# Optimization experiments

Hardware: AMD Instinct MI355X
Metric: run time of the kernel (lower is better)

The kernel has to match this reference:

```python
import jax, jax.numpy as jnp
import numpy as np

B, S, E, HEADS, LATENT = 8, 4096, 2048, 16, 64
HEAD_SIZE = E // HEADS  # 128
NEG = -1e20


def setup_inputs() -> dict:
    key = jax.random.key(0)
    k0, k1, k2, k3, k4 = jax.random.split(key, 5)
    return {
        "x": jax.random.normal(k0, (B, S, E), dtype=jnp.float32) * 0.02,
        "W_dkv": jax.random.normal(k1, (LATENT, E), dtype=jnp.float32) * 0.02,
        "W_k": jax.random.normal(k2, (HEAD_SIZE, LATENT), dtype=jnp.float32) * 0.02,
        "W_v": jax.random.normal(k3, (HEAD_SIZE, LATENT), dtype=jnp.float32) * 0.02,
        "W_q": jax.random.normal(k4, (HEAD_SIZE, E), dtype=jnp.float32) * 0.02,
    }


def reference(x, W_dkv, W_k, W_v, W_q):
    # x: [B,S,E]; nn.Linear computes x @ W.T (weight layout [out,in])
    head_size = W_k.shape[0]
    latent = jnp.einsum("bse,le->bsl", x, W_dkv)        # latent KV cache [B,S,L]
    absorbed_q = W_q.T @ W_k                              # [E,H] @ [H,L] -> [E,L]
    q_res = jnp.einsum("bse,el->bsl", x, absorbed_q)     # [B,S,L]
    scale = head_size ** -0.5
    scores = jnp.einsum("bql,bkl->bqk", q_res, latent) * scale  # [B,S,S]
    seq = x.shape[1]
    causal = jnp.tril(jnp.ones((seq, seq), dtype=bool))
    scores = jnp.where(causal, scores, NEG)
    attn = jax.nn.softmax(scores, axis=-1)               # dropout skipped (eval mode)
    v = jnp.einsum("bsl,hl->bsh", latent, W_v)           # compressed V [B,S,H]
    out = jnp.einsum("bqk,bkh->bqh", attn, v)            # [B,S,head_size]
    return out, latent  # latent == kv_cache returned by the module
```

## Files before the change

kernel.cpp:

```cpp
#include <hip/hip_runtime.h>
#include <hip/hip_bf16.h>

#define NB 8
#define NS 4096
#define NE 2048
#define NL 64
#define NH 128
#define NM (NB*NS)

typedef unsigned short ushort_t;
typedef __attribute__((ext_vector_type(4))) float f32x4;
typedef __attribute__((ext_vector_type(8))) __bf16 bf16x8;
typedef __attribute__((ext_vector_type(8))) unsigned short u16x8;
typedef __attribute__((ext_vector_type(4))) unsigned short u16x4;

#define SCALE2 0.1275174537f

__device__ __forceinline__ float fast_exp2(float x) {
    return __builtin_amdgcn_exp2f(x);
}

__device__ __forceinline__ unsigned short f2bf(float f) {
    union { float f; unsigned u; } v; v.f = f;
    unsigned u = v.u + 0x7fffu + ((v.u >> 16) & 1u);
    return (unsigned short)(u >> 16);
}

__device__ __forceinline__ float bf2f(ushort_t u) {
    union { unsigned u; float f; } v; v.u = (unsigned)u << 16; return v.f;
}

__device__ __forceinline__ int swz(int row, int colbyte) {
    return (row * 128 + colbyte) ^ ((row & 7) << 4);
}

__device__ __forceinline__ void wg_barrier() {
    asm volatile("s_waitcnt lgkmcnt(0)" ::: "memory");
    __builtin_amdgcn_s_barrier();
    __builtin_amdgcn_sched_barrier(0);
}

__global__ __launch_bounds__(256) void prep_kernel(
    const float* __restrict__ Wdkv, const float* __restrict__ Wk,
    const float* __restrict__ Wq, ushort_t* __restrict__ WcatT)
{
    __shared__ float wk[128 * 64];
    const int t = threadIdx.x;
    for (int i = t; i < 128 * 64; i += 256) wk[i] = Wk[i];
    __syncthreads();
    const int e = blockIdx.x * 256 + t;
    const int l0 = blockIdx.y * 16;
    float acc[16];
    #pragma unroll
    for (int l = 0; l < 16; ++l) acc[l] = 0.f;
    for (int h = 0; h < 128; ++h) {
        float q = Wq[h * NE + e];
        #pragma unroll
        for (int l = 0; l < 16; ++l) acc[l] += q * wk[h * 64 + l0 + l];
    }
    for (int l = 0; l < 16; ++l) WcatT[(64 + l0 + l) * NE + e] = f2bf(acc[l] * SCALE2);
    for (int l = 0; l < 16; ++l) WcatT[(l0 + l) * NE + e] = f2bf(Wdkv[(l0 + l) * NE + e]);
}

__global__ __launch_bounds__(256) void proj_kernel(
    const float* __restrict__ x, const ushort_t* __restrict__ WcatT,
    float* __restrict__ latent_out, ushort_t* __restrict__ k_bf,
    ushort_t* __restrict__ q_bf, ushort_t* __restrict__ kt)
{
    __shared__ ushort_t As[2][64 * 64];
    __shared__ ushort_t Bs[2][128 * 64];
    const int tid = threadIdx.x;
    const int w = tid >> 6, lane = tid & 63, lg = lane >> 4, li = lane & 15;
    const int m0 = blockIdx.x * 64;
    const int wm = (w >> 1) * 32, wn = (w & 1) * 64;
    const int srow = tid >> 3, scol = tid & 7;

    f32x4 acc[2][4];
    #pragma unroll
    for (int i = 0; i < 2; ++i)
        #pragma unroll
        for (int j = 0; j < 4; ++j) acc[i][j] = f32x4{0.f, 0.f, 0.f, 0.f};

    f32x4 a0reg[2][2], a1reg[2][2];
    u16x8 b0reg[4], b1reg[4];

#define PLOAD(k0, AR, BR) do { \
    _Pragma("unroll") for (int p = 0; p < 2; ++p) { \
        const float* gp = x + (long)(m0 + srow + 32 * p) * NE + (k0) + scol * 8; \
        AR[p][0] = *reinterpret_cast<const f32x4*>(gp); \
        AR[p][1] = *reinterpret_cast<const f32x4*>(gp + 4); } \
    _Pragma("unroll") for (int p = 0; p < 4; ++p) \
        BR[p] = *reinterpret_cast<const u16x8*>(WcatT + (long)(srow + 32 * p) * NE + (k0) + scol * 8); \
} while (0)

#define PWRITE(AR, BR, buf) do { \
    _Pragma("unroll") for (int p = 0; p < 2; ++p) { \
        union { unsigned uw[4]; u16x8 v; } hu; \
        asm("v_cvt_pk_bf16_f32 %0, %1, %2" : "=v"(hu.uw[0]) : "v"(AR[p][0][0]), "v"(AR[p][0][1])); \
        asm("v_cvt_pk_bf16_f32 %0, %1, %2" : "=v"(hu.uw[1]) : "v"(AR[p][0][2]), "v"(AR[p][0][3])); \
        asm("v_cvt_pk_bf16_f32 %0, %1, %2" : "=v"(hu.uw[2]) : "v"(AR[p][1][0]), "v"(AR[p][1][1])); \
        asm("v_cvt_pk_bf16_f32 %0, %1, %2" : "=v"(hu.uw[3]) : "v"(AR[p][1][2]), "v"(AR[p][1][3])); \
        *reinterpret_cast<u16x8*>(reinterpret_cast<char*>(As[buf]) + swz(srow + 32 * p, scol * 16)) = hu.v; } \
    _Pragma("unroll") for (int p = 0; p < 4; ++p) \
        *reinterpret_cast<u16x8*>(reinterpret_cast<char*>(Bs[buf]) + swz(srow + 32 * p, scol * 16)) = BR[p]; \
} while (0)

    auto compute = [&](int buf) {
        #pragma unroll
        for (int c = 0; c < 2; ++c) {
            bf16x8 af[2], bfv[4];
            #pragma unroll
            for (int mf = 0; mf < 2; ++mf)
                af[mf] = *reinterpret_cast<const bf16x8*>(
                    reinterpret_cast<const char*>(As[buf]) + swz(wm + 16 * mf + li, c * 64 + lg * 16));
            #pragma unroll
            for (int nf = 0; nf < 4; ++nf)
                bfv[nf] = *reinterpret_cast<const bf16x8*>(
                    reinterpret_cast<const char*>(Bs[buf]) + swz(wn + 16 * nf + li, c * 64 + lg * 16));
            #pragma unroll
            for (int mf = 0; mf < 2; ++mf)
                #pragma unroll
                for (int nf = 0; nf < 4; ++nf)
                    acc[mf][nf] = __builtin_amdgcn_mfma_f32_16x16x32_bf16(
                        af[mf], bfv[nf], acc[mf][nf], 0, 0, 0);
        }
    };

    PLOAD(0, a0reg, b0reg);
    PLOAD(64, a1reg, b1reg);
    PWRITE(a0reg, b0reg, 0);
    wg_barrier();

    for (int ks = 0; ks < 32; ks += 2) {
        if (ks + 2 < 32) PLOAD((ks + 2) * 64, a0reg, b0reg);
        compute(0);
        PWRITE(a1reg, b1reg, 1);
        wg_barrier();
        if (ks + 3 < 32) PLOAD((ks + 3) * 64, a1reg, b1reg);
        compute(1);
        if (ks + 2 < 32) PWRITE(a0reg, b0reg, 0);
        wg_barrier();
    }

    const int b = m0 >> 12, s0 = m0 & 4095;
    #pragma unroll
    for (int mf = 0; mf < 2; ++mf) {
        #pragma unroll
        for (int nf = 0; nf < 4; ++nf) {
            int col = wn + 16 * nf + li;
            #pragma unroll
            for (int r = 0; r < 4; ++r) {
                int row = m0 + wm + 16 * mf + 4 * lg + r;
                float v = acc[mf][nf][r];
                if (wn == 0) {
                    latent_out[(long)row * NL + col] = v;
                    k_bf[(long)row * NL + col] = f2bf(v);
                    *reinterpret_cast<ushort_t*>(reinterpret_cast<char*>(As[0]) +
                        swz(wm + 16 * mf + 4 * lg + r, col * 2)) = f2bf(v);
                } else {
                    q_bf[(long)row * NL + (col - 64)] = f2bf(v);
                }
            }
        }
    }
    wg_barrier();
    union { u16x8 u; bf16x8 v; } iu;
    #pragma unroll
    for (int j = 0; j < 8; ++j)
        iu.u[j] = (lg == (li >> 3) + 2 * (w & 1) && (li & 7) == j)
                      ? (ushort_t)0x3F80 : (ushort_t)0;
    const int ckt = w >> 1;
    f32x4 ktacc[4];
    #pragma unroll
    for (int nf = 0; nf < 4; ++nf) {
        bf16x8 bfv = *reinterpret_cast<const bf16x8*>(
            reinterpret_cast<const char*>(As[0]) + swz(16 * nf + li, ckt * 64 + lg * 16));
        ktacc[nf] = __builtin_amdgcn_mfma_f32_16x16x32_bf16(
            iu.v, bfv, f32x4{0.f, 0.f, 0.f, 0.f}, 0, 0, 0);
    }
    #pragma unroll
    for (int nf = 0; nf < 4; ++nf)
        #pragma unroll
        for (int r = 0; r < 4; ++r)
            kt[(long)(b * 64 + 16 * w + 4 * lg + r) * NS + s0 + 16 * nf + li] =
                f2bf(ktacc[nf][r]);
}

__global__ __launch_bounds__(256, 2) void attn_kernel(
    const ushort_t* __restrict__ q_bf, const ushort_t* __restrict__ k_bf,
    const ushort_t* __restrict__ kt, const float* __restrict__ Wv,
    float* __restrict__ out)
{
    __shared__ __attribute__((aligned(16))) char smem[65536];
    ushort_t* OW = (ushort_t*)smem;
    float* mw = (float*)(smem + 32768);
    float* lw = (float*)(smem + 33792);
    ushort_t* Ms = (ushort_t*)(smem + 36864);
    ushort_t* Wvs = (ushort_t*)(smem + 45056);
    float* Os = (float*)smem;

    const int tid = threadIdx.x;
    const int w = tid >> 6, lane = tid & 63, lg = lane >> 4, li = lane & 15;
    const int l = blockIdx.x;
    const int b = l & 7;
    const int p_ = l >> 3;
    const int k_ = p_ >> 1, e_ = p_ & 1, kk = (k_ & 15) * 2;
    const int qt = (k_ >> 4) ? (e_ ? kk + 1 : 63 - kk) : (e_ ? 62 - kk : kk);
    const int Q0 = qt << 6;
    const int nch = (qt >> 1) + 1;

    const int krow = tid >> 1, khalf = tid & 1;
    const int trow = tid >> 2, tkq = (tid & 3) * 32;

    bf16x8 qf[4][2];
    #pragma unroll
    for (int qb = 0; qb < 4; ++qb)
        #pragma unroll
        for (int c = 0; c < 2; ++c)
            qf[qb][c] = *reinterpret_cast<const bf16x8*>(
                q_bf + ((long)b * NS + Q0 + 16 * qb + li) * NL + c * 32 + lg * 8);

    float m_r[4], l_r[4];
    #pragma unroll
    for (int qb = 0; qb < 4; ++qb) { m_r[qb] = -1.0e30f; l_r[qb] = 0.f; }
    f32x4 oacc[4][4];
    #pragma unroll
    for (int qb = 0; qb < 4; ++qb)
        #pragma unroll
        for (int n = 0; n < 4; ++n) oacc[qb][n] = f32x4{0.f, 0.f, 0.f, 0.f};

    u16x8 k0reg[4], t0reg[4], k1reg[4], t1reg[4];

#define ALOAD(ch, KR, TR) do { \
    const int kv0_ = (ch) * 128; \
    _Pragma("unroll") for (int pp = 0; pp < 4; ++pp) \
        KR[pp] = *reinterpret_cast<const u16x8*>( \
            k_bf + ((long)b * NS + kv0_ + krow) * NL + khalf * 32 + pp * 8); \
    _Pragma("unroll") for (int pp = 0; pp < 4; ++pp) \
        TR[pp] = *reinterpret_cast<const u16x8*>( \
            kt + ((long)b * 64 + trow) * NS + kv0_ + tkq + pp * 8); \
} while (0)

#define AWRITE(KR, TR, buf) do { \
    char* Kb_ = smem + (buf) * 16384; \
    char* Tb_ = smem + 32768 + (buf) * 16384; \
    _Pragma("unroll") for (int pp = 0; pp < 4; ++pp) \
        *reinterpret_cast<u16x8*>(Kb_ + swz(krow, khalf * 64 + pp * 16)) = KR[pp]; \
    _Pragma("unroll") for (int pp = 0; pp < 4; ++pp) { \
        const int kv8 = tkq + pp * 8; \
        const int colp = (kv8 & 0x60) | ((kv8 & 0xC) << 1) | ((kv8 & 0x10) >> 2); \
        const int xo = (trow & 15) << 4; \
        u16x4 lo = {TR[pp][0], TR[pp][1], TR[pp][2], TR[pp][3]}; \
        u16x4 hi = {TR[pp][4], TR[pp][5], TR[pp][6], TR[pp][7]}; \
        *reinterpret_cast<u16x4*>(Tb_ + trow * 256 + ((colp * 2) ^ xo)) = lo; \
        *reinterpret_cast<u16x4*>(Tb_ + trow * 256 + (((colp + 8) * 2) ^ xo)) = hi; \
    } \
} while (0)

    auto compute = [&](int buf, bool diag, int kv0) {
        const char* Kb = smem + buf * 16384;
        const char* Tb = smem + 32768 + buf * 16384;
        f32x4 s[2][4];
        #pragma unroll
        for (int kvb = 0; kvb < 2; ++kvb)
            #pragma unroll
            for (int qb = 0; qb < 4; ++qb) s[kvb][qb] = f32x4{0.f, 0.f, 0.f, 0.f};
        __builtin_amdgcn_s_setprio(1);
        #pragma unroll
        for (int c = 0; c < 2; ++c)
            #pragma unroll
            for (int kvb = 0; kvb < 2; ++kvb) {
                bf16x8 a = *reinterpret_cast<const bf16x8*>(
                    Kb + swz(32 * w + 16 * kvb + li, c * 64 + lg * 16));
                #pragma unroll
                for (int qb = 0; qb < 4; ++qb)
                    s[kvb][qb] = __builtin_amdgcn_mfma_f32_16x16x32_bf16(
                        a, qf[qb][c], s[kvb][qb], 0, 0, 0);
            }
        __builtin_amdgcn_s_setprio(0);
        if (diag) {
            #pragma unroll
            for (int kvb = 0; kvb < 2; ++kvb)
                #pragma unroll
                for (int qb = 0; qb < 4; ++qb)
                    #pragma unroll
                    for (int r = 0; r < 4; ++r) {
                        int kv_g = kv0 + 32 * w + 16 * kvb + 4 * lg + r;
                        int q_g = Q0 + 16 * qb + li;
                        if (kv_g > q_g) s[kvb][qb][r] = -3.0e38f;
                    }
        }
        float mx[4];
        #pragma unroll
        for (int qb = 0; qb < 4; ++qb) {
            float m0_ = fmaxf(fmaxf(s[0][qb][0], s[0][qb][1]), fmaxf(s[0][qb][2], s[0][qb][3]));
            float m1_ = fmaxf(fmaxf(s[1][qb][0], s[1][qb][1]), fmaxf(s[1][qb][2], s[1][qb][3]));
            mx[qb] = fmaxf(m0_, m1_);
        }
        bool ok = (mx[0] <= m_r[0] + 8.f) && (mx[1] <= m_r[1] + 8.f) &&
                  (mx[2] <= m_r[2] + 8.f) && (mx[3] <= m_r[3] + 8.f);
        if (!__all(ok)) {
            #pragma unroll
            for (int qb = 0; qb < 4; ++qb) {
                float mxf = fmaxf(mx[qb], __shfl_xor(mx[qb], 16));
                mxf = fmaxf(mxf, __shfl_xor(mxf, 32));
                float m_new = fmaxf(m_r[qb], mxf);
                float corr = fast_exp2(m_r[qb] - m_new);
                m_r[qb] = m_new;
                l_r[qb] *= corr;
                float corrO[4];
                #pragma unroll
                for (int r = 0; r < 4; ++r)
                    corrO[r] = __shfl(corr, (lane & 48) | (4 * lg + r));
                #pragma unroll
                for (int n = 0; n < 4; ++n)
                    #pragma unroll
                    for (int r = 0; r < 4; ++r) oacc[qb][n][r] *= corrO[r];
            }
        }
        #pragma unroll
        for (int qb = 0; qb < 4; ++qb) {
            float rs = 0.f;
            #pragma unroll
            for (int kvb = 0; kvb < 2; ++kvb)
                #pragma unroll
                for (int r = 0; r < 4; ++r) {
                    float pv = fast_exp2(s[kvb][qb][r] - m_r[qb]);
                    s[kvb][qb][r] = pv;
                    rs += pv;
                }
            l_r[qb] += rs;
        }
        bf16x8 vb[4];
        #pragma unroll
        for (int n = 0; n < 4; ++n)
            vb[n] = *reinterpret_cast<const bf16x8*>(
                Tb + (16 * n + li) * 256 + ((64 * w + 16 * lg) ^ (li << 4)));
        __builtin_amdgcn_s_setprio(1);
        #pragma unroll
        for (int qb = 0; qb < 4; ++qb) {
            union { unsigned uw[4]; bf16x8 v; } pa;
            asm("v_cvt_pk_bf16_f32 %0, %1, %2" : "=v"(pa.uw[0]) : "v"(s[0][qb][0]), "v"(s[0][qb][1]));
            asm("v_cvt_pk_bf16_f32 %0, %1, %2" : "=v"(pa.uw[1]) : "v"(s[0][qb][2]), "v"(s[0][qb][3]));
            asm("v_cvt_pk_bf16_f32 %0, %1, %2" : "=v"(pa.uw[2]) : "v"(s[1][qb][0]), "v"(s[1][qb][1]));
            asm("v_cvt_pk_bf16_f32 %0, %1, %2" : "=v"(pa.uw[3]) : "v"(s[1][qb][2]), "v"(s[1][qb][3]));
            #pragma unroll
            for (int n = 0; n < 4; ++n)
                oacc[qb][n] = __builtin_amdgcn_mfma_f32_16x16x32_bf16(
                    pa.v, vb[n], oacc[qb][n], 0, 0, 0);
        }
        __builtin_amdgcn_s_setprio(0);
    };

    ALOAD(0, k0reg, t0reg);
    if (nch >= 2) ALOAD(1, k1reg, t1reg);
    AWRITE(k0reg, t0reg, 0);
    wg_barrier();
    for (int i = 0; i < nch; i += 2) {
        if (i + 2 < nch) ALOAD(i + 2, k0reg, t0reg);
        compute(0, i == nch - 1, i * 128);
        if (i + 1 < nch) AWRITE(k1reg, t1reg, 1);
        wg_barrier();
        if (i + 1 >= nch) break;
        if (i + 3 < nch) ALOAD(i + 3, k1reg, t1reg);
        compute(1, i + 1 == nch - 1, (i + 1) * 128);
        if (i + 2 < nch) AWRITE(k0reg, t0reg, 0);
        wg_barrier();
    }

    #pragma unroll
    for (int qb = 0; qb < 4; ++qb) {
        l_r[qb] += __shfl_xor(l_r[qb], 16);
        l_r[qb] += __shfl_xor(l_r[qb], 32);
    }
    if (lg == 0) {
        #pragma unroll
        for (int qb = 0; qb < 4; ++qb) {
            mw[w * 64 + 16 * qb + li] = m_r[qb];
            lw[w * 64 + 16 * qb + li] = l_r[qb];
        }
    }
    #pragma unroll
    for (int qb = 0; qb < 4; ++qb)
        #pragma unroll
        for (int r = 0; r < 4; ++r) {
            union { unsigned uw[2]; u16x4 v; } u;
            asm("v_cvt_pk_bf16_f32 %0, %1, %2" : "=v"(u.uw[0]) : "v"(oacc[qb][0][r]), "v"(oacc[qb][1][r]));
            asm("v_cvt_pk_bf16_f32 %0, %1, %2" : "=v"(u.uw[1]) : "v"(oacc[qb][2][r]), "v"(oacc[qb][3][r]));
            int q = 16 * qb + 4 * lg + r;
            *reinterpret_cast<u16x4*>(OW + (w * 64 + q) * 64 + li * 4) = u.v;
        }
    wg_barrier();

    {
        const int q = tid >> 2, g = tid & 3;
        float m4[4], l4[4];
        #pragma unroll
        for (int ww = 0; ww < 4; ++ww) { m4[ww] = mw[ww * 64 + q]; l4[ww] = lw[ww * 64 + q]; }
        float M = fmaxf(fmaxf(m4[0], m4[1]), fmaxf(m4[2], m4[3]));
        float cw[4], L = 0.f;
        #pragma unroll
        for (int ww = 0; ww < 4; ++ww) { cw[ww] = fast_exp2(m4[ww] - M); L += cw[ww] * l4[ww]; }
        float inv = 1.f / L;
        float merged[16];
        #pragma unroll
        for (int e = 0; e < 16; ++e) {
            float a = 0.f;
            #pragma unroll
            for (int ww = 0; ww < 4; ++ww)
                a += cw[ww] * bf2f(OW[(ww * 64 + q) * 64 + e * 4 + g]);
            merged[e] = a * inv;
        }
        #pragma unroll
        for (int ee = 0; ee < 8; ++ee) {
            unsigned pk;
            asm("v_cvt_pk_bf16_f32 %0, %1, %2" : "=v"(pk) : "v"(merged[2 * ee]), "v"(merged[2 * ee + 1]));
            *reinterpret_cast<unsigned*>(reinterpret_cast<char*>(Ms) + swz(q, g * 32 + 4 * ee)) = pk;
        }
        const int r = tid >> 1, hf = tid & 1;
        const float* wp = Wv + r * 64 + hf * 32;
        #pragma unroll
        for (int qq = 0; qq < 2; ++qq) {
            f32x4 w0 = *reinterpret_cast<const f32x4*>(wp + qq * 16);
            f32x4 w1 = *reinterpret_cast<const f32x4*>(wp + qq * 16 + 4);
            f32x4 w2 = *reinterpret_cast<const f32x4*>(wp + qq * 16 + 8);
            f32x4 w3 = *reinterpret_cast<const f32x4*>(wp + qq * 16 + 12);
            u16x8 h0, h1;
            #pragma unroll
            for (int jj = 0; jj < 4; ++jj) {
                h0[jj] = f2bf(w0[jj]); h0[4 + jj] = f2bf(w1[jj]);
                h1[jj] = f2bf(w2[jj]); h1[4 + jj] = f2bf(w3[jj]);
            }
            *reinterpret_cast<u16x8*>(reinterpret_cast<char*>(Wvs) + swz(r, hf * 64 + qq * 32)) = h0;
            *reinterpret_cast<u16x8*>(reinterpret_cast<char*>(Wvs) + swz(r, hf * 64 + qq * 32 + 16)) = h1;
        }
    }
    wg_barrier();

    f32x4 vacc[2][4];
    #pragma unroll
    for (int i = 0; i < 2; ++i)
        #pragma unroll
        for (int j = 0; j < 4; ++j) vacc[i][j] = f32x4{0.f, 0.f, 0.f, 0.f};
    #pragma unroll
    for (int c = 0; c < 2; ++c) {
        bf16x8 af[2], bfv[4];
        #pragma unroll
        for (int mf = 0; mf < 2; ++mf)
            af[mf] = *reinterpret_cast<const bf16x8*>(
                reinterpret_cast<const char*>(Wvs) + swz(32 * w + 16 * mf + li, c * 64 + lg * 16));
        #pragma unroll
        for (int nf = 0; nf < 4; ++nf)
            bfv[nf] = *reinterpret_cast<const bf16x8*>(
                reinterpret_cast<const char*>(Ms) + swz(16 * nf + li, c * 64 + lg * 16));
        #pragma unroll
        for (int mf = 0; mf < 2; ++mf)
            #pragma unroll
            for (int nf = 0; nf < 4; ++nf)
                vacc[mf][nf] = __builtin_amdgcn_mfma_f32_16x16x32_bf16(
                    af[mf], bfv[nf], vacc[mf][nf], 0, 0, 0);
    }
    wg_barrier();
    #pragma unroll
    for (int mf = 0; mf < 2; ++mf)
        #pragma unroll
        for (int nf = 0; nf < 4; ++nf)
            #pragma unroll
            for (int r = 0; r < 4; ++r)
                Os[(16 * nf + li) * 132 + 32 * w + 16 * mf + 4 * lg + r] = vacc[mf][nf][r];
    wg_barrier();
    {
        const int r = tid >> 2, cb = (tid & 3) * 32;
        float* op = out + ((long)b * NS + Q0 + r) * NH + cb;
        const float* sp = Os + r * 132 + cb;
        #pragma unroll
        for (int qq = 0; qq < 8; ++qq)
            *reinterpret_cast<f32x4*>(op + 4 * qq) = *reinterpret_cast<const f32x4*>(sp + 4 * qq);
    }
}

extern "C" void kernel_launch(void* const* d_in, const int* in_sizes, int n_in,
                              void* d_out, int out_size, void* d_ws, size_t ws_size,
                              hipStream_t stream) {
    const float* x    = (const float*)d_in[0];
    const float* Wdkv = (const float*)d_in[1];
    const float* Wk   = (const float*)d_in[2];
    const float* Wv   = (const float*)d_in[3];
    const float* Wq   = (const float*)d_in[4];

    float* out = (float*)d_out;
    float* latent_out = out + (long)NM * NH;

    ushort_t* WcatT = (ushort_t*)d_ws;
    ushort_t* q_bf  = WcatT + 128 * NE;
    ushort_t* k_bf  = q_bf + (long)NM * NL;
    ushort_t* kt    = k_bf + (long)NM * NL;

    hipLaunchKernelGGL(prep_kernel, dim3(NE / 256, 4), dim3(256), 0, stream, Wdkv, Wk, Wq, WcatT);
    hipLaunchKernelGGL(proj_kernel, dim3(NM / 64), dim3(256), 0, stream,
                       x, WcatT, latent_out, k_bf, q_bf, kt);
    hipLaunchKernelGGL(attn_kernel, dim3(512), dim3(256), 0, stream,
                       q_bf, k_bf, kt, Wv, out);
}
```

Measured before the change: 133.4 us.

## Load K fragments directly into registers, drop K and Wv LDS staging

```diff
diff --git a/kernel.cpp b/kernel.cpp
--- a/kernel.cpp
+++ b/kernel.cpp
@@ -191,12 +191,11 @@
     const ushort_t* __restrict__ kt, const float* __restrict__ Wv,
     float* __restrict__ out)
 {
-    __shared__ __attribute__((aligned(16))) char smem[65536];
+    __shared__ __attribute__((aligned(16))) char smem[45056];
     ushort_t* OW = (ushort_t*)smem;
     float* mw = (float*)(smem + 32768);
     float* lw = (float*)(smem + 33792);
     ushort_t* Ms = (ushort_t*)(smem + 36864);
-    ushort_t* Wvs = (ushort_t*)(smem + 45056);
     float* Os = (float*)smem;
 
     const int tid = threadIdx.x;
@@ -209,7 +208,6 @@
     const int Q0 = qt << 6;
     const int nch = (qt >> 1) + 1;
 
-    const int krow = tid >> 1, khalf = tid & 1;
     const int trow = tid >> 2, tkq = (tid & 3) * 32;
 
     bf16x8 qf[4][2];
@@ -229,37 +227,39 @@
         #pragma unroll
         for (int n = 0; n < 4; ++n) oacc[qb][n] = f32x4{0.f, 0.f, 0.f, 0.f};
 
-    u16x8 k0reg[4], t0reg[4], k1reg[4], t1reg[4];
-
-#define ALOAD(ch, KR, TR) do { \
+    bf16x8 kfA[2][2], kfB[2][2];
+    u16x8 treg[4];
+
+#define KLOAD(ch, KF) do { \
+    const int kv0_ = (ch) * 128; \
+    _Pragma("unroll") for (int c = 0; c < 2; ++c) \
+        _Pragma("unroll") for (int kvb = 0; kvb < 2; ++kvb) \
+            KF[c][kvb] = *reinterpret_cast<const bf16x8*>( \
+                k_bf + ((long)b * NS + kv0_ + 32 * w + 16 * kvb + li) * NL + c * 32 + lg * 8); \
+} while (0)
+
+#define TLOAD(ch) do { \
     const int kv0_ = (ch) * 128; \
     _Pragma("unroll") for (int pp = 0; pp < 4; ++pp) \
-        KR[pp] = *reinterpret_cast<const u16x8*>( \
-            k_bf + ((long)b * NS + kv0_ + krow) * NL + khalf * 32 + pp * 8); \
-    _Pragma("unroll") for (int pp = 0; pp < 4; ++pp) \
-        TR[pp] = *reinterpret_cast<const u16x8*>( \
+        treg[pp] = *reinterpret_cast<const u16x8*>( \
             kt + ((long)b * 64 + trow) * NS + kv0_ + tkq + pp * 8); \
 } while (0)
 
-#define AWRITE(KR, TR, buf) do { \
-    char* Kb_ = smem + (buf) * 16384; \
-    char* Tb_ = smem + 32768 + (buf) * 16384; \
-    _Pragma("unroll") for (int pp = 0; pp < 4; ++pp) \
-        *reinterpret_cast<u16x8*>(Kb_ + swz(krow, khalf * 64 + pp * 16)) = KR[pp]; \
+#define TWRITE(buf) do { \
+    char* Tb_ = smem + (buf) * 16384; \
     _Pragma("unroll") for (int pp = 0; pp < 4; ++pp) { \
         const int kv8 = tkq + pp * 8; \
         const int colp = (kv8 & 0x60) | ((kv8 & 0xC) << 1) | ((kv8 & 0x10) >> 2); \
         const int xo = (trow & 15) << 4; \
-        u16x4 lo = {TR[pp][0], TR[pp][1], TR[pp][2], TR[pp][3]}; \
-        u16x4 hi = {TR[pp][4], TR[pp][5], TR[pp][6], TR[pp][7]}; \
+        u16x4 lo = {treg[pp][0], treg[pp][1], treg[pp][2], treg[pp][3]}; \
+        u16x4 hi = {treg[pp][4], treg[pp][5], treg[pp][6], treg[pp][7]}; \
         *reinterpret_cast<u16x4*>(Tb_ + trow * 256 + ((colp * 2) ^ xo)) = lo; \
         *reinterpret_cast<u16x4*>(Tb_ + trow * 256 + (((colp + 8) * 2) ^ xo)) = hi; \
     } \
 } while (0)
 
-    auto compute = [&](int buf, bool diag, int kv0) {
-        const char* Kb = smem + buf * 16384;
-        const char* Tb = smem + 32768 + buf * 16384;
+    auto compute = [&](int buf, bool diag, int kv0, bf16x8 (&kf)[2][2]) {
+        const char* Tb = smem + buf * 16384;
         f32x4 s[2][4];
         #pragma unroll
         for (int kvb = 0; kvb < 2; ++kvb)
@@ -270,12 +270,10 @@
         for (int c = 0; c < 2; ++c)
             #pragma unroll
             for (int kvb = 0; kvb < 2; ++kvb) {
-                bf16x8 a = *reinterpret_cast<const bf16x8*>(
-                    Kb + swz(32 * w + 16 * kvb + li, c * 64 + lg * 16));
                 #pragma unroll
                 for (int qb = 0; qb < 4; ++qb)
                     s[kvb][qb] = __builtin_amdgcn_mfma_f32_16x16x32_bf16(
-                        a, qf[qb][c], s[kvb][qb], 0, 0, 0);
+                        kf[c][kvb], qf[qb][c], s[kvb][qb], 0, 0, 0);
             }
         __builtin_amdgcn_s_setprio(0);
         if (diag) {
@@ -352,21 +350,42 @@
         __builtin_amdgcn_s_setprio(0);
     };
 
-    ALOAD(0, k0reg, t0reg);
-    if (nch >= 2) ALOAD(1, k1reg, t1reg);
-    AWRITE(k0reg, t0reg, 0);
-    wg_barrier();
+    KLOAD(0, kfA);
+    TLOAD(0);
+    if (nch >= 2) KLOAD(1, kfB);
+    TWRITE(0);
+    if (nch >= 2) TLOAD(1);
+    wg_barrier();
+
     for (int i = 0; i < nch; i += 2) {
-        if (i + 2 < nch) ALOAD(i + 2, k0reg, t0reg);
-        compute(0, i == nch - 1, i * 128);
-        if (i + 1 < nch) AWRITE(k1reg, t1reg, 1);
+        compute(0, i == nch - 1, i * 128, kfA);
+        if (i + 2 < nch) KLOAD(i + 2, kfA);
+        if (i + 1 < nch) TWRITE(1);
+        if (i + 2 < nch) TLOAD(i + 2);
         wg_barrier();
         if (i + 1 >= nch) break;
-        if (i + 3 < nch) ALOAD(i + 3, k1reg, t1reg);
-        compute(1, i + 1 == nch - 1, (i + 1) * 128);
-        if (i + 2 < nch) AWRITE(k0reg, t0reg, 0);
+        compute(1, i + 1 == nch - 1, (i + 1) * 128, kfB);
+        if (i + 3 < nch) KLOAD(i + 3, kfB);
+        if (i + 2 < nch) TWRITE(0);
+        if (i + 3 < nch) TLOAD(i + 3);
         wg_barrier();
     }
+
+    bf16x8 waf[2][2];
+    #pragma unroll
+    for (int c = 0; c < 2; ++c)
+        #pragma unroll
+        for (int mf = 0; mf < 2; ++mf) {
+            const float* wp_ = Wv + (32 * w + 16 * mf + li) * 64 + c * 32 + lg * 8;
+            f32x4 wa = *reinterpret_cast<const f32x4*>(wp_);
+            f32x4 wb = *reinterpret_cast<const f32x4*>(wp_ + 4);
+            union { unsigned uw[4]; bf16x8 v; } hu;
+            asm("v_cvt_pk_bf16_f32 %0, %1, %2" : "=v"(hu.uw[0]) : "v"(wa[0]), "v"(wa[1]));
+            asm("v_cvt_pk_bf16_f32 %0, %1, %2" : "=v"(hu.uw[1]) : "v"(wa[2]), "v"(wa[3]));
+            asm("v_cvt_pk_bf16_f32 %0, %1, %2" : "=v"(hu.uw[2]) : "v"(wb[0]), "v"(wb[1]));
+            asm("v_cvt_pk_bf16_f32 %0, %1, %2" : "=v"(hu.uw[3]) : "v"(wb[2]), "v"(wb[3]));
+            waf[c][mf] = hu.v;
+        }
 
     #pragma unroll
     for (int qb = 0; qb < 4; ++qb) {
@@ -417,23 +436,6 @@
             asm("v_cvt_pk_bf16_f32 %0, %1, %2" : "=v"(pk) : "v"(merged[2 * ee]), "v"(merged[2 * ee + 1]));
             *reinterpret_cast<unsigned*>(reinterpret_cast<char*>(Ms) + swz(q, g * 32 + 4 * ee)) = pk;
         }
-        const int r = tid >> 1, hf = tid & 1;
-        const float* wp = Wv + r * 64 + hf * 32;
-        #pragma unroll
-        for (int qq = 0; qq < 2; ++qq) {
-            f32x4 w0 = *reinterpret_cast<const f32x4*>(wp + qq * 16);
-            f32x4 w1 = *reinterpret_cast<const f32x4*>(wp + qq * 16 + 4);
-            f32x4 w2 = *reinterpret_cast<const f32x4*>(wp + qq * 16 + 8);
-            f32x4 w3 = *reinterpret_cast<const f32x4*>(wp + qq * 16 + 12);
-            u16x8 h0, h1;
-            #pragma unroll
-            for (int jj = 0; jj < 4; ++jj) {
-                h0[jj] = f2bf(w0[jj]); h0[4 + jj] = f2bf(w1[jj]);
-                h1[jj] = f2bf(w2[jj]); h1[4 + jj] = f2bf(w3[jj]);
-            }
-            *reinterpret_cast<u16x8*>(reinterpret_cast<char*>(Wvs) + swz(r, hf * 64 + qq * 32)) = h0;
-            *reinterpret_cast<u16x8*>(reinterpret_cast<char*>(Wvs) + swz(r, hf * 64 + qq * 32 + 16)) = h1;
-        }
     }
     wg_barrier();
 
@@ -444,11 +446,7 @@
         for (int j = 0; j < 4; ++j) vacc[i][j] = f32x4{0.f, 0.f, 0.f, 0.f};
     #pragma unroll
     for (int c = 0; c < 2; ++c) {
-        bf16x8 af[2], bfv[4];
-        #pragma unroll
-        for (int mf = 0; mf < 2; ++mf)
-            af[mf] = *reinterpret_cast<const bf16x8*>(
-                reinterpret_cast<const char*>(Wvs) + swz(32 * w + 16 * mf + li, c * 64 + lg * 16));
+        bf16x8 bfv[4];
         #pragma unroll
         for (int nf = 0; nf < 4; ++nf)
             bfv[nf] = *reinterpret_cast<const bf16x8*>(
@@ -458,7 +456,7 @@
             #pragma unroll
             for (int nf = 0; nf < 4; ++nf)
                 vacc[mf][nf] = __builtin_amdgcn_mfma_f32_16x16x32_bf16(
-                    af[mf], bfv[nf], vacc[mf][nf], 0, 0, 0);
+                    waf[c][mf], bfv[nf], vacc[mf][nf], 0, 0, 0);
     }
     wg_barrier();
     #pragma unroll
```

New measurement: 139.5 us. +4.6%, slower.

## Split causal KV range across two blocks and add a separate merge kernel

Applied to the files above, without the earlier changes.

```diff
diff --git a/kernel.cpp b/kernel.cpp
--- a/kernel.cpp
+++ b/kernel.cpp
@@ -188,26 +188,23 @@
 
 __global__ __launch_bounds__(256, 2) void attn_kernel(
     const ushort_t* __restrict__ q_bf, const ushort_t* __restrict__ k_bf,
-    const ushort_t* __restrict__ kt, const float* __restrict__ Wv,
-    float* __restrict__ out)
+    const ushort_t* __restrict__ kt, unsigned* __restrict__ Opart,
+    float* __restrict__ lpart, float* __restrict__ mpart)
 {
     __shared__ __attribute__((aligned(16))) char smem[65536];
     ushort_t* OW = (ushort_t*)smem;
     float* mw = (float*)(smem + 32768);
     float* lw = (float*)(smem + 33792);
-    ushort_t* Ms = (ushort_t*)(smem + 36864);
-    ushort_t* Wvs = (ushort_t*)(smem + 45056);
-    float* Os = (float*)smem;
 
     const int tid = threadIdx.x;
     const int w = tid >> 6, lane = tid & 63, lg = lane >> 4, li = lane & 15;
-    const int l = blockIdx.x;
-    const int b = l & 7;
-    const int p_ = l >> 3;
-    const int k_ = p_ >> 1, e_ = p_ & 1, kk = (k_ & 15) * 2;
-    const int qt = (k_ >> 4) ? (e_ ? kk + 1 : 63 - kk) : (e_ ? 62 - kk : kk);
+    const int j = blockIdx.x;
+    const int qt = 63 - (j >> 4);
+    const int b = j & 7;
+    const int h = (j >> 3) & 1;
     const int Q0 = qt << 6;
-    const int nch = (qt >> 1) + 1;
+    const int ntot = (qt >> 1) + 1;
+    const int nch = (ntot - h + 1) >> 1;
 
     const int krow = tid >> 1, khalf = tid & 1;
     const int trow = tid >> 2, tkq = (tid & 3) * 32;
@@ -352,20 +349,24 @@
         __builtin_amdgcn_s_setprio(0);
     };
 
-    ALOAD(0, k0reg, t0reg);
-    if (nch >= 2) ALOAD(1, k1reg, t1reg);
-    AWRITE(k0reg, t0reg, 0);
-    wg_barrier();
-    for (int i = 0; i < nch; i += 2) {
-        if (i + 2 < nch) ALOAD(i + 2, k0reg, t0reg);
-        compute(0, i == nch - 1, i * 128);
-        if (i + 1 < nch) AWRITE(k1reg, t1reg, 1);
+    if (nch > 0) {
+        ALOAD(h, k0reg, t0reg);
+        if (nch >= 2) ALOAD(h + 2, k1reg, t1reg);
+        AWRITE(k0reg, t0reg, 0);
         wg_barrier();
-        if (i + 1 >= nch) break;
-        if (i + 3 < nch) ALOAD(i + 3, k1reg, t1reg);
-        compute(1, i + 1 == nch - 1, (i + 1) * 128);
-        if (i + 2 < nch) AWRITE(k0reg, t0reg, 0);
-        wg_barrier();
+        for (int i = 0; i < nch; i += 2) {
+            const int c0_ = h + 2 * i;
+            if (i + 2 < nch) ALOAD(h + 2 * (i + 2), k0reg, t0reg);
+            compute(0, c0_ == ntot - 1, c0_ * 128);
+            if (i + 1 < nch) AWRITE(k1reg, t1reg, 1);
+            wg_barrier();
+            if (i + 1 >= nch) break;
+            const int c1_ = h + 2 * (i + 1);
+            if (i + 3 < nch) ALOAD(h + 2 * (i + 3), k1reg, t1reg);
+            compute(1, c1_ == ntot - 1, c1_ * 128);
+            if (i + 2 < nch) AWRITE(k0reg, t0reg, 0);
+            wg_barrier();
+        }
     }
 
     #pragma unroll
@@ -401,20 +402,66 @@
         float cw[4], L = 0.f;
         #pragma unroll
         for (int ww = 0; ww < 4; ++ww) { cw[ww] = fast_exp2(m4[ww] - M); L += cw[ww] * l4[ww]; }
-        float inv = 1.f / L;
-        float merged[16];
+        float numer[16];
         #pragma unroll
         for (int e = 0; e < 16; ++e) {
             float a = 0.f;
             #pragma unroll
             for (int ww = 0; ww < 4; ++ww)
                 a += cw[ww] * bf2f(OW[(ww * 64 + q) * 64 + e * 4 + g]);
-            merged[e] = a * inv;
-        }
+            numer[e] = a;
+        }
+        const long P = ((long)(h * NB + b) << 6) + qt;
+        unsigned* op = Opart + P * 2048 + q * 32 + g * 8;
         #pragma unroll
         for (int ee = 0; ee < 8; ++ee) {
             unsigned pk;
-            asm("v_cvt_pk_bf16_f32 %0, %1, %2" : "=v"(pk) : "v"(merged[2 * ee]), "v"(merged[2 * ee + 1]));
+            asm("v_cvt_pk_bf16_f32 %0, %1, %2" : "=v"(pk) : "v"(numer[2 * ee]), "v"(numer[2 * ee + 1]));
+            op[ee] = pk;
+        }
+        if (g == 0) {
+            lpart[P * 64 + q] = L;
+            mpart[P * 64 + q] = M;
+        }
+    }
+}
+
+__global__ __launch_bounds__(256) void merge_kernel(
+    const unsigned* __restrict__ Opart, const float* __restrict__ lpart,
+    const float* __restrict__ mpart, const float* __restrict__ Wv,
+    float* __restrict__ out)
+{
+    __shared__ __attribute__((aligned(16))) char smem[33792];
+    ushort_t* Ms = (ushort_t*)smem;
+    ushort_t* Wvs = (ushort_t*)(smem + 8192);
+    float* Os = (float*)smem;
+    const int blk = blockIdx.x;
+    const int b = blk & 7, qt = blk >> 3;
+    const int tid = threadIdx.x;
+    const int w = tid >> 6, lane = tid & 63, lg = lane >> 4, li = lane & 15;
+
+    {
+        const int q = tid >> 2, g = tid & 3;
+        const long P1 = ((long)b << 6) + qt;
+        const long P2 = ((long)(NB + b) << 6) + qt;
+        float l1 = lpart[P1 * 64 + q], m1 = mpart[P1 * 64 + q];
+        float l2 = lpart[P2 * 64 + q], m2 = mpart[P2 * 64 + q];
+        float M = fmaxf(m1, m2);
+        float w1 = fast_exp2(m1 - M), w2 = fast_exp2(m2 - M);
+        float inv = 1.f / (w1 * l1 + w2 * l2);
+        float a1 = w1 * inv, a2 = w2 * inv;
+        const unsigned* o1 = Opart + P1 * 2048 + q * 32 + g * 8;
+        const unsigned* o2 = Opart + P2 * 2048 + q * 32 + g * 8;
+        #pragma unroll
+        for (int ee = 0; ee < 8; ++ee) {
+            unsigned u1 = o1[ee], u2 = o2[ee];
+            union { unsigned u; float f; } c0, c1, d0, d1;
+            c0.u = u1 << 16; c1.u = u1 & 0xffff0000u;
+            d0.u = u2 << 16; d1.u = u2 & 0xffff0000u;
+            float rlo = a1 * c0.f + a2 * d0.f;
+            float rhi = a1 * c1.f + a2 * d1.f;
+            unsigned pk;
+            asm("v_cvt_pk_bf16_f32 %0, %1, %2" : "=v"(pk) : "v"(rlo), "v"(rhi));
             *reinterpret_cast<unsigned*>(reinterpret_cast<char*>(Ms) + swz(q, g * 32 + 4 * ee)) = pk;
         }
         const int r = tid >> 1, hf = tid & 1;
@@ -422,14 +469,14 @@
         #pragma unroll
         for (int qq = 0; qq < 2; ++qq) {
             f32x4 w0 = *reinterpret_cast<const f32x4*>(wp + qq * 16);
-            f32x4 w1 = *reinterpret_cast<const f32x4*>(wp + qq * 16 + 4);
-            f32x4 w2 = *reinterpret_cast<const f32x4*>(wp + qq * 16 + 8);
+            f32x4 wv1 = *reinterpret_cast<const f32x4*>(wp + qq * 16 + 4);
+            f32x4 w2v = *reinterpret_cast<const f32x4*>(wp + qq * 16 + 8);
             f32x4 w3 = *reinterpret_cast<const f32x4*>(wp + qq * 16 + 12);
             u16x8 h0, h1;
             #pragma unroll
             for (int jj = 0; jj < 4; ++jj) {
-                h0[jj] = f2bf(w0[jj]); h0[4 + jj] = f2bf(w1[jj]);
-                h1[jj] = f2bf(w2[jj]); h1[4 + jj] = f2bf(w3[jj]);
+                h0[jj] = f2bf(w0[jj]); h0[4 + jj] = f2bf(wv1[jj]);
+                h1[jj] = f2bf(w2v[jj]); h1[4 + jj] = f2bf(w3[jj]);
             }
             *reinterpret_cast<u16x8*>(reinterpret_cast<char*>(Wvs) + swz(r, hf * 64 + qq * 32)) = h0;
             *reinterpret_cast<u16x8*>(reinterpret_cast<char*>(Wvs) + swz(r, hf * 64 + qq * 32 + 16)) = h1;
@@ -441,7 +488,7 @@
     #pragma unroll
     for (int i = 0; i < 2; ++i)
         #pragma unroll
-        for (int j = 0; j < 4; ++j) vacc[i][j] = f32x4{0.f, 0.f, 0.f, 0.f};
+        for (int jj = 0; jj < 4; ++jj) vacc[i][jj] = f32x4{0.f, 0.f, 0.f, 0.f};
     #pragma unroll
     for (int c = 0; c < 2; ++c) {
         bf16x8 af[2], bfv[4];
@@ -471,7 +518,7 @@
     wg_barrier();
     {
         const int r = tid >> 2, cb = (tid & 3) * 32;
-        float* op = out + ((long)b * NS + Q0 + r) * NH + cb;
+        float* op = out + ((long)b * NS + qt * 64 + r) * NH + cb;
         const float* sp = Os + r * 132 + cb;
         #pragma unroll
         for (int qq = 0; qq < 8; ++qq)
@@ -495,10 +542,15 @@
     ushort_t* q_bf  = WcatT + 128 * NE;
     ushort_t* k_bf  = q_bf + (long)NM * NL;
     ushort_t* kt    = k_bf + (long)NM * NL;
+    unsigned* Opart = (unsigned*)(kt + (long)NM * NL);
+    float* lpart = (float*)(Opart + (long)1024 * 2048);
+    float* mpart = lpart + 1024 * 64;
 
     hipLaunchKernelGGL(prep_kernel, dim3(NE / 256, 4), dim3(256), 0, stream, Wdkv, Wk, Wq, WcatT);
     hipLaunchKernelGGL(proj_kernel, dim3(NM / 64), dim3(256), 0, stream,
                        x, WcatT, latent_out, k_bf, q_bf, kt);
-    hipLaunchKernelGGL(attn_kernel, dim3(512), dim3(256), 0, stream,
-                       q_bf, k_bf, kt, Wv, out);
-}
+    hipLaunchKernelGGL(attn_kernel, dim3(1024), dim3(256), 0, stream,
+                       q_bf, k_bf, kt, Opart, lpart, mpart);
+    hipLaunchKernelGGL(merge_kernel, dim3(512), dim3(256), 0, stream,
+                       Opart, lpart, mpart, Wv, out);
+}
```

After: 139.9 us. 1.05x slower.

## Split attention into LDS-free per-wave KV partitions with separate merge kernel

Applied to the files above, without the earlier changes.

```diff
diff --git a/kernel.cpp b/kernel.cpp
--- a/kernel.cpp
+++ b/kernel.cpp
@@ -13,6 +13,7 @@
 typedef __attribute__((ext_vector_type(8))) __bf16 bf16x8;
 typedef __attribute__((ext_vector_type(8))) unsigned short u16x8;
 typedef __attribute__((ext_vector_type(4))) unsigned short u16x4;
+typedef __attribute__((ext_vector_type(4))) unsigned int u32x4;
 
 #define SCALE2 0.1275174537f
 
@@ -186,122 +187,93 @@
                 f2bf(ktacc[nf][r]);
 }
 
-__global__ __launch_bounds__(256, 2) void attn_kernel(
+__global__ __launch_bounds__(256, 3) void attn_kernel(
     const ushort_t* __restrict__ q_bf, const ushort_t* __restrict__ k_bf,
-    const ushort_t* __restrict__ kt, const float* __restrict__ Wv,
-    float* __restrict__ out)
+    const ushort_t* __restrict__ kt, unsigned* __restrict__ Opart,
+    float* __restrict__ lpart, float* __restrict__ mpart)
 {
-    __shared__ __attribute__((aligned(16))) char smem[65536];
-    ushort_t* OW = (ushort_t*)smem;
-    float* mw = (float*)(smem + 32768);
-    float* lw = (float*)(smem + 33792);
-    ushort_t* Ms = (ushort_t*)(smem + 36864);
-    ushort_t* Wvs = (ushort_t*)(smem + 45056);
-    float* Os = (float*)smem;
-
     const int tid = threadIdx.x;
     const int w = tid >> 6, lane = tid & 63, lg = lane >> 4, li = lane & 15;
-    const int l = blockIdx.x;
-    const int b = l & 7;
-    const int p_ = l >> 3;
-    const int k_ = p_ >> 1, e_ = p_ & 1, kk = (k_ & 15) * 2;
-    const int qt = (k_ >> 4) ? (e_ ? kk + 1 : 63 - kk) : (e_ ? 62 - kk : kk);
-    const int Q0 = qt << 6;
-    const int nch = (qt >> 1) + 1;
-
-    const int krow = tid >> 1, khalf = tid & 1;
-    const int trow = tid >> 2, tkq = (tid & 3) * 32;
-
-    bf16x8 qf[4][2];
-    #pragma unroll
-    for (int qb = 0; qb < 4; ++qb)
+    const int j = blockIdx.x;
+    const int t = 127 - (j >> 3);
+    const int b = j & 7;
+    const int h = w;
+    const int Q0 = t << 5;
+    const int nch = (h <= t) ? ((t - h) >> 2) + 1 : 0;
+
+    bf16x8 qf[2][2];
+    #pragma unroll
+    for (int qb = 0; qb < 2; ++qb)
         #pragma unroll
         for (int c = 0; c < 2; ++c)
             qf[qb][c] = *reinterpret_cast<const bf16x8*>(
                 q_bf + ((long)b * NS + Q0 + 16 * qb + li) * NL + c * 32 + lg * 8);
 
-    float m_r[4], l_r[4];
-    #pragma unroll
-    for (int qb = 0; qb < 4; ++qb) { m_r[qb] = -1.0e30f; l_r[qb] = 0.f; }
-    f32x4 oacc[4][4];
-    #pragma unroll
-    for (int qb = 0; qb < 4; ++qb)
+    float m_r[2], l_r[2];
+    m_r[0] = m_r[1] = -1.0e30f;
+    l_r[0] = l_r[1] = 0.f;
+    f32x4 oacc[2][4];
+    #pragma unroll
+    for (int qb = 0; qb < 2; ++qb)
         #pragma unroll
         for (int n = 0; n < 4; ++n) oacc[qb][n] = f32x4{0.f, 0.f, 0.f, 0.f};
 
-    u16x8 k0reg[4], t0reg[4], k1reg[4], t1reg[4];
-
-#define ALOAD(ch, KR, TR) do { \
-    const int kv0_ = (ch) * 128; \
-    _Pragma("unroll") for (int pp = 0; pp < 4; ++pp) \
-        KR[pp] = *reinterpret_cast<const u16x8*>( \
-            k_bf + ((long)b * NS + kv0_ + krow) * NL + khalf * 32 + pp * 8); \
-    _Pragma("unroll") for (int pp = 0; pp < 4; ++pp) \
-        TR[pp] = *reinterpret_cast<const u16x8*>( \
-            kt + ((long)b * 64 + trow) * NS + kv0_ + tkq + pp * 8); \
-} while (0)
-
-#define AWRITE(KR, TR, buf) do { \
-    char* Kb_ = smem + (buf) * 16384; \
-    char* Tb_ = smem + 32768 + (buf) * 16384; \
-    _Pragma("unroll") for (int pp = 0; pp < 4; ++pp) \
-        *reinterpret_cast<u16x8*>(Kb_ + swz(krow, khalf * 64 + pp * 16)) = KR[pp]; \
-    _Pragma("unroll") for (int pp = 0; pp < 4; ++pp) { \
-        const int kv8 = tkq + pp * 8; \
-        const int colp = (kv8 & 0x60) | ((kv8 & 0xC) << 1) | ((kv8 & 0x10) >> 2); \
-        const int xo = (trow & 15) << 4; \
-        u16x4 lo = {TR[pp][0], TR[pp][1], TR[pp][2], TR[pp][3]}; \
-        u16x4 hi = {TR[pp][4], TR[pp][5], TR[pp][6], TR[pp][7]}; \
-        *reinterpret_cast<u16x4*>(Tb_ + trow * 256 + ((colp * 2) ^ xo)) = lo; \
-        *reinterpret_cast<u16x4*>(Tb_ + trow * 256 + (((colp + 8) * 2) ^ xo)) = hi; \
+    union VB { u16x4 h4[2]; bf16x8 v; };
+    bf16x8 kfA[2][2], kfB[2][2];
+    VB vbA[4], vbB[4];
+
+#define AKLOAD(ch, KF, VBv) do { \
+    const int kv0_ = (ch) * 32; \
+    _Pragma("unroll") for (int c = 0; c < 2; ++c) \
+        _Pragma("unroll") for (int f = 0; f < 2; ++f) \
+            KF[c][f] = *reinterpret_cast<const bf16x8*>( \
+                k_bf + ((long)b * NS + kv0_ + 16 * f + li) * NL + c * 32 + lg * 8); \
+    _Pragma("unroll") for (int n = 0; n < 4; ++n) { \
+        const ushort_t* kp_ = kt + ((long)b * 64 + 16 * n + li) * NS + kv0_ + 4 * lg; \
+        VBv[n].h4[0] = *reinterpret_cast<const u16x4*>(kp_); \
+        VBv[n].h4[1] = *reinterpret_cast<const u16x4*>(kp_ + 16); \
     } \
 } while (0)
 
-    auto compute = [&](int buf, bool diag, int kv0) {
-        const char* Kb = smem + buf * 16384;
-        const char* Tb = smem + 32768 + buf * 16384;
-        f32x4 s[2][4];
-        #pragma unroll
-        for (int kvb = 0; kvb < 2; ++kvb)
-            #pragma unroll
-            for (int qb = 0; qb < 4; ++qb) s[kvb][qb] = f32x4{0.f, 0.f, 0.f, 0.f};
+    auto compute = [&](bf16x8 (&kf)[2][2], VB (&vb)[4], bool diag, int kv0) {
+        f32x4 s[2][2];
+        #pragma unroll
+        for (int f = 0; f < 2; ++f)
+            #pragma unroll
+            for (int qb = 0; qb < 2; ++qb) s[f][qb] = f32x4{0.f, 0.f, 0.f, 0.f};
         __builtin_amdgcn_s_setprio(1);
         #pragma unroll
         for (int c = 0; c < 2; ++c)
             #pragma unroll
-            for (int kvb = 0; kvb < 2; ++kvb) {
-                bf16x8 a = *reinterpret_cast<const bf16x8*>(
-                    Kb + swz(32 * w + 16 * kvb + li, c * 64 + lg * 16));
+            for (int f = 0; f < 2; ++f)
                 #pragma unroll
-                for (int qb = 0; qb < 4; ++qb)
-                    s[kvb][qb] = __builtin_amdgcn_mfma_f32_16x16x32_bf16(
-                        a, qf[qb][c], s[kvb][qb], 0, 0, 0);
-            }
+                for (int qb = 0; qb < 2; ++qb)
+                    s[f][qb] = __builtin_amdgcn_mfma_f32_16x16x32_bf16(
+                        kf[c][f], qf[qb][c], s[f][qb], 0, 0, 0);
         __builtin_amdgcn_s_setprio(0);
         if (diag) {
             #pragma unroll
-            for (int kvb = 0; kvb < 2; ++kvb)
+            for (int f = 0; f < 2; ++f)
                 #pragma unroll
-                for (int qb = 0; qb < 4; ++qb)
+                for (int qb = 0; qb < 2; ++qb)
                     #pragma unroll
                     for (int r = 0; r < 4; ++r) {
-                        int kv_g = kv0 + 32 * w + 16 * kvb + 4 * lg + r;
+                        int kv_g = kv0 + 16 * f + 4 * lg + r;
                         int q_g = Q0 + 16 * qb + li;
-                        if (kv_g > q_g) s[kvb][qb][r] = -3.0e38f;
+                        if (kv_g > q_g) s[f][qb][r] = -3.0e38f;
                     }
         }
-        float mx[4];
-        #pragma unroll
-        for (int qb = 0; qb < 4; ++qb) {
+        float mx[2];
+        #pragma unroll
+        for (int qb = 0; qb < 2; ++qb) {
             float m0_ = fmaxf(fmaxf(s[0][qb][0], s[0][qb][1]), fmaxf(s[0][qb][2], s[0][qb][3]));
             float m1_ = fmaxf(fmaxf(s[1][qb][0], s[1][qb][1]), fmaxf(s[1][qb][2], s[1][qb][3]));
             mx[qb] = fmaxf(m0_, m1_);
         }
-        bool ok = (mx[0] <= m_r[0] + 8.f) && (mx[1] <= m_r[1] + 8.f) &&
-                  (mx[2] <= m_r[2] + 8.f) && (mx[3] <= m_r[3] + 8.f);
+        bool ok = (mx[0] <= m_r[0] + 8.f) && (mx[1] <= m_r[1] + 8.f);
         if (!__all(ok)) {
             #pragma unroll
-            for (int qb = 0; qb < 4; ++qb) {
+            for (int qb = 0; qb < 2; ++qb) {
                 float mxf = fmaxf(mx[qb], __shfl_xor(mx[qb], 16));
                 mxf = fmaxf(mxf, __shfl_xor(mxf, 32));
                 float m_new = fmaxf(m_r[qb], mxf);
@@ -319,26 +291,21 @@
             }
         }
         #pragma unroll
-        for (int qb = 0; qb < 4; ++qb) {
+        for (int qb = 0; qb < 2; ++qb) {
             float rs = 0.f;
             #pragma unroll
-            for (int kvb = 0; kvb < 2; ++kvb)
+            for (int f = 0; f < 2; ++f)
                 #pragma unroll
                 for (int r = 0; r < 4; ++r) {
-                    float pv = fast_exp2(s[kvb][qb][r] - m_r[qb]);
-                    s[kvb][qb][r] = pv;
+                    float pv = fast_exp2(s[f][qb][r] - m_r[qb]);
+                    s[f][qb][r] = pv;
                     rs += pv;
                 }
             l_r[qb] += rs;
         }
-        bf16x8 vb[4];
-        #pragma unroll
-        for (int n = 0; n < 4; ++n)
-            vb[n] = *reinterpret_cast<const bf16x8*>(
-                Tb + (16 * n + li) * 256 + ((64 * w + 16 * lg) ^ (li << 4)));
         __builtin_amdgcn_s_setprio(1);
         #pragma unroll
-        for (int qb = 0; qb < 4; ++qb) {
+        for (int qb = 0; qb < 2; ++qb) {
             union { unsigned uw[4]; bf16x8 v; } pa;
             asm("v_cvt_pk_bf16_f32 %0, %1, %2" : "=v"(pa.uw[0]) : "v"(s[0][qb][0]), "v"(s[0][qb][1]));
             asm("v_cvt_pk_bf16_f32 %0, %1, %2" : "=v"(pa.uw[1]) : "v"(s[0][qb][2]), "v"(s[0][qb][3]));
@@ -347,75 +314,100 @@
             #pragma unroll
             for (int n = 0; n < 4; ++n)
                 oacc[qb][n] = __builtin_amdgcn_mfma_f32_16x16x32_bf16(
-                    pa.v, vb[n], oacc[qb][n], 0, 0, 0);
+                    pa.v, vb[n].v, oacc[qb][n], 0, 0, 0);
         }
         __builtin_amdgcn_s_setprio(0);
     };
 
-    ALOAD(0, k0reg, t0reg);
-    if (nch >= 2) ALOAD(1, k1reg, t1reg);
-    AWRITE(k0reg, t0reg, 0);
-    wg_barrier();
-    for (int i = 0; i < nch; i += 2) {
-        if (i + 2 < nch) ALOAD(i + 2, k0reg, t0reg);
-        compute(0, i == nch - 1, i * 128);
-        if (i + 1 < nch) AWRITE(k1reg, t1reg, 1);
-        wg_barrier();
-        if (i + 1 >= nch) break;
-        if (i + 3 < nch) ALOAD(i + 3, k1reg, t1reg);
-        compute(1, i + 1 == nch - 1, (i + 1) * 128);
-        if (i + 2 < nch) AWRITE(k0reg, t0reg, 0);
-        wg_barrier();
-    }
-
-    #pragma unroll
-    for (int qb = 0; qb < 4; ++qb) {
+    if (nch > 0) {
+        AKLOAD(h, kfA, vbA);
+        for (int i = 0; i < nch; i += 2) {
+            if (i + 1 < nch) AKLOAD(h + 4 * (i + 1), kfB, vbB);
+            compute(kfA, vbA, h + 4 * i == t, (h + 4 * i) * 32);
+            if (i + 1 >= nch) break;
+            if (i + 2 < nch) AKLOAD(h + 4 * (i + 2), kfA, vbA);
+            compute(kfB, vbB, h + 4 * (i + 1) == t, (h + 4 * (i + 1)) * 32);
+        }
+    }
+
+    #pragma unroll
+    for (int qb = 0; qb < 2; ++qb) {
         l_r[qb] += __shfl_xor(l_r[qb], 16);
         l_r[qb] += __shfl_xor(l_r[qb], 32);
     }
-    if (lg == 0) {
-        #pragma unroll
-        for (int qb = 0; qb < 4; ++qb) {
-            mw[w * 64 + 16 * qb + li] = m_r[qb];
-            lw[w * 64 + 16 * qb + li] = l_r[qb];
-        }
-    }
-    #pragma unroll
-    for (int qb = 0; qb < 4; ++qb)
+    const long P = ((long)(h * NB + b) << 7) + t;
+    #pragma unroll
+    for (int qb = 0; qb < 2; ++qb)
         #pragma unroll
         for (int r = 0; r < 4; ++r) {
             union { unsigned uw[2]; u16x4 v; } u;
             asm("v_cvt_pk_bf16_f32 %0, %1, %2" : "=v"(u.uw[0]) : "v"(oacc[qb][0][r]), "v"(oacc[qb][1][r]));
             asm("v_cvt_pk_bf16_f32 %0, %1, %2" : "=v"(u.uw[1]) : "v"(oacc[qb][2][r]), "v"(oacc[qb][3][r]));
             int q = 16 * qb + 4 * lg + r;
-            *reinterpret_cast<u16x4*>(OW + (w * 64 + q) * 64 + li * 4) = u.v;
-        }
-    wg_barrier();
+            *reinterpret_cast<u16x4*>(Opart + P * 1024 + q * 32 + li * 2) = u.v;
+        }
+    if (lg == 0) {
+        #pragma unroll
+        for (int qb = 0; qb < 2; ++qb) {
+            lpart[P * 32 + 16 * qb + li] = l_r[qb];
+            mpart[P * 32 + 16 * qb + li] = m_r[qb];
+        }
+    }
+}
+
+__global__ __launch_bounds__(256) void merge_kernel(
+    const unsigned* __restrict__ Opart, const float* __restrict__ lpart,
+    const float* __restrict__ mpart, const float* __restrict__ Wv,
+    float* __restrict__ out)
+{
+    __shared__ __attribute__((aligned(16))) char smem[20992];
+    ushort_t* Ms = (ushort_t*)smem;
+    ushort_t* Wvs = (ushort_t*)(smem + 4096);
+    float* Os = (float*)smem;
+    const int blk = blockIdx.x;
+    const int b = blk & 7, t = blk >> 3;
+    const int Q0 = t << 5;
+    const int tid = threadIdx.x;
+    const int w = tid >> 6, lane = tid & 63, lg = lane >> 4, li = lane & 15;
 
     {
-        const int q = tid >> 2, g = tid & 3;
-        float m4[4], l4[4];
-        #pragma unroll
-        for (int ww = 0; ww < 4; ++ww) { m4[ww] = mw[ww * 64 + q]; l4[ww] = lw[ww * 64 + q]; }
+        const int q = tid >> 3, g = tid & 7;
+        float l4[4], m4[4];
+        #pragma unroll
+        for (int hh = 0; hh < 4; ++hh) {
+            const long P = ((long)(hh * NB + b) << 7) + t;
+            l4[hh] = lpart[P * 32 + q];
+            m4[hh] = mpart[P * 32 + q];
+        }
         float M = fmaxf(fmaxf(m4[0], m4[1]), fmaxf(m4[2], m4[3]));
-        float cw[4], L = 0.f;
-        #pragma unroll
-        for (int ww = 0; ww < 4; ++ww) { cw[ww] = fast_exp2(m4[ww] - M); L += cw[ww] * l4[ww]; }
+        float a[4], L = 0.f;
+        #pragma unroll
+        for (int hh = 0; hh < 4; ++hh) { a[hh] = fast_exp2(m4[hh] - M); L += a[hh] * l4[hh]; }
         float inv = 1.f / L;
-        float merged[16];
-        #pragma unroll
-        for (int e = 0; e < 16; ++e) {
-            float a = 0.f;
-            #pragma unroll
-            for (int ww = 0; ww < 4; ++ww)
-                a += cw[ww] * bf2f(OW[(ww * 64 + q) * 64 + e * 4 + g]);
-            merged[e] = a * inv;
-        }
-        #pragma unroll
-        for (int ee = 0; ee < 8; ++ee) {
-            unsigned pk;
-            asm("v_cvt_pk_bf16_f32 %0, %1, %2" : "=v"(pk) : "v"(merged[2 * ee]), "v"(merged[2 * ee + 1]));
-            *reinterpret_cast<unsigned*>(reinterpret_cast<char*>(Ms) + swz(q, g * 32 + 4 * ee)) = pk;
+        #pragma unroll
+        for (int hh = 0; hh < 4; ++hh) a[hh] *= inv;
+        float acc[8];
+        #pragma unroll
+        for (int k = 0; k < 8; ++k) acc[k] = 0.f;
+        #pragma unroll
+        for (int hh = 0; hh < 4; ++hh) {
+            const long P = ((long)(hh * NB + b) << 7) + t;
+            u32x4 v = *reinterpret_cast<const u32x4*>(Opart + P * 1024 + q * 32 + g * 4);
+            #pragma unroll
+            for (int k = 0; k < 4; ++k) {
+                union { unsigned u; float f; } lo, hi;
+                lo.u = v[k] << 16; hi.u = v[k] & 0xffff0000u;
+                acc[2 * k]     += a[hh] * lo.f;
+                acc[2 * k + 1] += a[hh] * hi.f;
+            }
+        }
+        #pragma unroll
+        for (int k = 0; k < 4; ++k) {
+            int u = g * 4 + k;
+            int li2 = u >> 1, p = u & 1;
+            int dlo = 32 * p + li2, dhi = dlo + 16;
+            *reinterpret_cast<ushort_t*>(reinterpret_cast<char*>(Ms) + swz(q, dlo * 2)) = f2bf(acc[2 * k]);
+            *reinterpret_cast<ushort_t*>(reinterpret_cast<char*>(Ms) + swz(q, dhi * 2)) = f2bf(acc[2 * k + 1]);
         }
         const int r = tid >> 1, hf = tid & 1;
         const float* wp = Wv + r * 64 + hf * 32;
@@ -437,26 +429,26 @@
     }
     wg_barrier();
 
-    f32x4 vacc[2][4];
+    f32x4 vacc[2][2];
     #pragma unroll
     for (int i = 0; i < 2; ++i)
         #pragma unroll
-        for (int j = 0; j < 4; ++j) vacc[i][j] = f32x4{0.f, 0.f, 0.f, 0.f};
+        for (int jj = 0; jj < 2; ++jj) vacc[i][jj] = f32x4{0.f, 0.f, 0.f, 0.f};
     #pragma unroll
     for (int c = 0; c < 2; ++c) {
-        bf16x8 af[2], bfv[4];
+        bf16x8 af[2], bfv[2];
         #pragma unroll
         for (int mf = 0; mf < 2; ++mf)
             af[mf] = *reinterpret_cast<const bf16x8*>(
                 reinterpret_cast<const char*>(Wvs) + swz(32 * w + 16 * mf + li, c * 64 + lg * 16));
         #pragma unroll
-        for (int nf = 0; nf < 4; ++nf)
+        for (int nf = 0; nf < 2; ++nf)
             bfv[nf] = *reinterpret_cast<const bf16x8*>(
                 reinterpret_cast<const char*>(Ms) + swz(16 * nf + li, c * 64 + lg * 16));
         #pragma unroll
         for (int mf = 0; mf < 2; ++mf)
             #pragma unroll
-            for (int nf = 0; nf < 4; ++nf)
+            for (int nf = 0; nf < 2; ++nf)
                 vacc[mf][nf] = __builtin_amdgcn_mfma_f32_16x16x32_bf16(
                     af[mf], bfv[nf], vacc[mf][nf], 0, 0, 0);
     }
@@ -464,17 +456,17 @@
     #pragma unroll
     for (int mf = 0; mf < 2; ++mf)
         #pragma unroll
-        for (int nf = 0; nf < 4; ++nf)
+        for (int nf = 0; nf < 2; ++nf)
             #pragma unroll
             for (int r = 0; r < 4; ++r)
                 Os[(16 * nf + li) * 132 + 32 * w + 16 * mf + 4 * lg + r] = vacc[mf][nf][r];
     wg_barrier();
     {
-        const int r = tid >> 2, cb = (tid & 3) * 32;
+        const int r = tid >> 3, cb = (tid & 7) * 16;
         float* op = out + ((long)b * NS + Q0 + r) * NH + cb;
         const float* sp = Os + r * 132 + cb;
         #pragma unroll
-        for (int qq = 0; qq < 8; ++qq)
+        for (int qq = 0; qq < 4; ++qq)
             *reinterpret_cast<f32x4*>(op + 4 * qq) = *reinterpret_cast<const f32x4*>(sp + 4 * qq);
     }
 }
@@ -495,10 +487,15 @@
     ushort_t* q_bf  = WcatT + 128 * NE;
     ushort_t* k_bf  = q_bf + (long)NM * NL;
     ushort_t* kt    = k_bf + (long)NM * NL;
+    unsigned* Opart = (unsigned*)(kt + (long)NM * NL);
+    float* lpart = (float*)(Opart + (long)4096 * 1024);
+    float* mpart = lpart + 4096 * 32;
 
     hipLaunchKernelGGL(prep_kernel, dim3(NE / 256, 4), dim3(256), 0, stream, Wdkv, Wk, Wq, WcatT);
     hipLaunchKernelGGL(proj_kernel, dim3(NM / 64), dim3(256), 0, stream,
                        x, WcatT, latent_out, k_bf, q_bf, kt);
-    hipLaunchKernelGGL(attn_kernel, dim3(512), dim3(256), 0, stream,
-                       q_bf, k_bf, kt, Wv, out);
-}
+    hipLaunchKernelGGL(attn_kernel, dim3(1024), dim3(256), 0, stream,
+                       q_bf, k_bf, kt, Opart, lpart, mpart);
+    hipLaunchKernelGGL(merge_kernel, dim3(1024), dim3(256), 0, stream,
+                       Opart, lpart, mpart, Wv, out);
+}
```

After: 200.0 us. +49.9%, slower.
